# Performance work log

Hardware: AMD Instinct MI355X
Metric: run time of the kernel (lower is better)

Reference implementation:

```python
import jax, jax.numpy as jnp
import numpy as np

LN_EPS = 1e-5  # torch.nn.LayerNorm default


def setup_inputs() -> dict:
    key = jax.random.key(0)
    k1, k2 = jax.random.split(key)
    N, D_IN, D_OUT, G = 4096, 512, 512, 32
    x = jax.random.normal(k1, (N, D_IN), dtype=jnp.float32)
    ln_w = jnp.ones((D_IN,), dtype=jnp.float32)
    ln_b = jnp.zeros((D_IN,), dtype=jnp.float32)
    scale = 1.0 / (np.sqrt(D_IN) * np.sqrt(G))
    fouriercoeffs = jax.random.normal(k2, (2, D_OUT, D_IN, G), dtype=jnp.float32) * scale
    bias = jnp.zeros((1, D_OUT), dtype=jnp.float32)
    return {"x": x, "ln_w": ln_w, "ln_b": ln_b, "fouriercoeffs": fouriercoeffs, "bias": bias}


def reference(x, ln_w, ln_b, fouriercoeffs, bias):
    # LayerNorm over last dim
    mu = jnp.mean(x, axis=-1, keepdims=True)
    var = jnp.mean((x - mu) ** 2, axis=-1, keepdims=True)
    xn = (x - mu) * jax.lax.rsqrt(var + LN_EPS) * ln_w + ln_b
    G = fouriercoeffs.shape[-1]
    k = jnp.arange(1, G + 1, dtype=xn.dtype)           # [G]
    arg = xn[:, :, None] * k                            # [N, D_in, G]
    c = jnp.cos(arg)
    s = jnp.sin(arg)
    # contraction over (inputdim, gridsize) -> GEMM-shaped einsum
    y = jnp.einsum('big,oig->bo', c, fouriercoeffs[0])
    y = y + jnp.einsum('big,oig->bo', s, fouriercoeffs[1])
    y = y + bias
    return y
```

## Files before the change

kernel.cpp:

```cpp
#include <hip/hip_runtime.h>
#include <hip/hip_bf16.h>


#define N_ROWS 4096
#define D_IN   512
#define D_OUT  512
#define KT     16384
#define BM 128
#define BN 128
#define SPLITK 4

typedef short short8 __attribute__((ext_vector_type(8)));
typedef float float4v __attribute__((ext_vector_type(4)));

__device__ inline unsigned int pack2bf(float a, float b) {
    __hip_bfloat162 h = __float22bfloat162_rn(make_float2(a, b));
    union { __hip_bfloat162 h; unsigned int u; } cv;
    cv.h = h;
    return cv.u;
}

__device__ inline unsigned short bf16_1(float a) {
    union { float f; unsigned int u; } cv;
    cv.f = a;
    unsigned int r = (cv.u + 0x7fff + ((cv.u >> 16) & 1)) >> 16;
    return (unsigned short)r;
}

__global__ __launch_bounds__(256) void ln_stats(const float* __restrict__ x,
        float2* __restrict__ mu_rs) {
    const int t = threadIdx.x;
    const int row = blockIdx.x * 4 + (t >> 6);
    const int lane = t & 63;
    const float4* xr = (const float4*)(x + (size_t)row * D_IN);
    float4 a = xr[lane];
    float4 c = xr[lane + 64];
    float s = a.x + a.y + a.z + a.w + c.x + c.y + c.z + c.w;
    float q = a.x * a.x + a.y * a.y + a.z * a.z + a.w * a.w
            + c.x * c.x + c.y * c.y + c.z * c.z + c.w * c.w;
    #pragma unroll
    for (int off = 32; off > 0; off >>= 1) {
        s += __shfl_down(s, off, 64);
        q += __shfl_down(q, off, 64);
    }
    if (lane == 0) {
        float mu = s * (1.f / D_IN);
        float var = q * (1.f / D_IN) - mu * mu;
        mu_rs[row] = make_float2(mu, rsqrtf(var + 1e-5f));
    }
}

__global__ __launch_bounds__(256) void feat_seed(const float* __restrict__ x,
        const float* __restrict__ w, const float* __restrict__ b,
        const float2* __restrict__ mu_rs, float2* __restrict__ csT) {
    __shared__ float2 tile[64][66];
    const int t = threadIdx.x;
    const int r0 = blockIdx.x * 64, i0 = blockIdx.y * 64;
    const int rr = t >> 6;
    const int cc = t & 63;
    const float wv = w[i0 + cc], bv = b[i0 + cc];
    #pragma unroll
    for (int p = 0; p < 16; ++p) {
        const int row = r0 + p * 4 + rr;
        float v = x[(size_t)row * D_IN + i0 + cc];
        float2 mr = mu_rs[row];
        float xn = (v - mr.x) * mr.y * wv + bv;
        float sn, cn;
        __sincosf(xn, &sn, &cn);
        tile[cc][p * 4 + rr] = make_float2(cn, sn);
    }
    __syncthreads();
    #pragma unroll
    for (int p = 0; p < 16; ++p) {
        const int dim = p * 4 + rr;
        csT[(size_t)(i0 + dim) * N_ROWS + r0 + cc] = tile[dim][cc];
    }
}

__global__ __launch_bounds__(256) void cvt_kernel(const float* __restrict__ fc,
        unsigned short* __restrict__ Wb) {
    size_t e = ((size_t)blockIdx.x * 256 + threadIdx.x) * 8;
    const float4* in = (const float4*)(fc + e);
    float4 a = in[0];
    float4 c = in[1];
    uint4 o;
    o.x = pack2bf(a.x, a.y);
    o.y = pack2bf(a.z, a.w);
    o.z = pack2bf(c.x, c.y);
    o.w = pack2bf(c.z, c.w);
    *(uint4*)(Wb + e) = o;
}

__device__ inline void stage_feats(unsigned short* Abuf, float2 cs, int ttype,
                                   int frow, int ihalf) {
    const float c1 = cs.x, s1 = cs.y;
    const float c2 = c1 + c1;
    float prev = ttype ? 0.f : 1.f;
    float cur  = ttype ? s1 : c1;
    const int rbase = frow * 64;
    const int sw = frow & 7;
    unsigned int us[4];
    #pragma unroll
    for (int d = 0; d < 16; ++d) {
        float f0 = cur;
        float f1 = __builtin_fmaf(c2, cur, -prev);
        float f2 = __builtin_fmaf(c2, f1, -cur);
        prev = f1;
        cur = f2;
        us[d & 3] = pack2bf(f0, f1);
        if ((d & 3) == 3) {
            const int kc = ihalf * 4 + (d >> 2);
            *(uint4*)&Abuf[rbase + ((kc ^ sw) << 3)] =
                make_uint4(us[0], us[1], us[2], us[3]);
        }
    }
}

__global__ __launch_bounds__(256, 2) void fkan_gemm(const float2* __restrict__ csT,
        const unsigned short* __restrict__ Wb, unsigned short* __restrict__ pb) {
    __shared__ unsigned short As[2][BM * 64];
    __shared__ unsigned short Bs[2][BN * 64];
    const int t = threadIdx.x;
    const int row0 = blockIdx.x * BM;
    const int col0 = blockIdx.y * BN;
    const int kz = blockIdx.z;
    const int k0 = kz * 4096;
    const int i0 = kz * 128;
    const int frow = t & 127;
    const int ihalf = t >> 7;
    const int l = t & 63, wv = t >> 6;
    const int wm = (wv & 1) * 64, wn = (wv >> 1) * 64;
    const int lm = l & 15, lq = l >> 4;
    const int c8 = l & 7, s8 = l >> 3;
    const unsigned short* Bg0 = Wb + (size_t)(col0 + wv * 32 + c8) * KT + k0 + s8 * 8;
    const int swA = lm & 7;
    const int bBase = ((wn >> 3) + (lm >> 3)) * 512 + lq * 64 + (lm & 7) * 8;

    const float2* csBase = csT + (size_t)(i0 + ihalf) * N_ROWS + row0 + frow;

    float4v acc[4][4];
    #pragma unroll
    for (int i = 0; i < 4; ++i)
        #pragma unroll
        for (int j = 0; j < 4; ++j)
            acc[i][j] = (float4v){0.f, 0.f, 0.f, 0.f};

    #pragma unroll
    for (int j = 0; j < 4; ++j) {
        const unsigned short* gsrc = Bg0 + (size_t)(j * 8) * KT;
        unsigned short* ldst = &Bs[0][(wv * 4 + j) * 512];
        __builtin_amdgcn_global_load_lds(
            (const __attribute__((address_space(1))) unsigned int*)gsrc,
            (__attribute__((address_space(3))) unsigned int*)ldst, 16, 0, 0);
    }
    float2 cs = csBase[0];
    stage_feats(As[0], cs, 0, frow, ihalf);
    cs = csBase[2 * N_ROWS];
    __syncthreads();

    for (int iter = 0; iter < 128; ++iter) {
        const int p = iter & 1;
        if (iter < 127) {
            const int in = iter + 1;
            const int tt = in >> 6, ii = in & 63;
            const unsigned short* gb = Bg0 + (size_t)tt * D_OUT * KT + ii * 64;
            #pragma unroll
            for (int j = 0; j < 4; ++j) {
                const unsigned short* gsrc = gb + (size_t)(j * 8) * KT;
                unsigned short* ldst = &Bs[p ^ 1][(wv * 4 + j) * 512];
                __builtin_amdgcn_global_load_lds(
                    (const __attribute__((address_space(1))) unsigned int*)gsrc,
                    (__attribute__((address_space(3))) unsigned int*)ldst, 16, 0, 0);
            }
            stage_feats(As[p ^ 1], cs, tt, frow, ihalf);
        }
        if (iter < 126)
            cs = csBase[(size_t)(((iter + 2) & 63) * 2) * N_ROWS];
        #pragma unroll
        for (int h = 0; h < 2; ++h) {
            short8 af[4], bf[4];
            #pragma unroll
            for (int tm = 0; tm < 4; ++tm)
                af[tm] = *(const short8*)
                    &As[p][(wm + tm * 16 + lm) * 64 + (((h * 4 + lq) ^ swA) << 3)];
            #pragma unroll
            for (int tn = 0; tn < 4; ++tn)
                bf[tn] = *(const short8*)&Bs[p][bBase + tn * 1024 + h * 256];
            #pragma unroll
            for (int tm = 0; tm < 4; ++tm)
                #pragma unroll
                for (int tn = 0; tn < 4; ++tn)
                    acc[tm][tn] = __builtin_amdgcn_mfma_f32_16x16x32_bf16(
                        af[tm], bf[tn], acc[tm][tn], 0, 0, 0);
        }
        __syncthreads();
    }
    unsigned short* pc = pb + (size_t)kz * N_ROWS * D_OUT;
    #pragma unroll
    for (int tm = 0; tm < 4; ++tm)
        #pragma unroll
        for (int tn = 0; tn < 4; ++tn)
            #pragma unroll
            for (int r = 0; r < 4; ++r) {
                const int row = row0 + wm + tm * 16 + lq * 4 + r;
                const int col = col0 + wn + tn * 16 + lm;
                pc[(size_t)row * D_OUT + col] = bf16_1(acc[tm][tn][r]);
            }
}

__global__ __launch_bounds__(256) void reduce_kernel(const unsigned short* __restrict__ pb,
        const float* __restrict__ bias, float* __restrict__ out) {
    const size_t e = ((size_t)blockIdx.x * 256 + threadIdx.x) * 4;
    const int col = (int)(e & (D_OUT - 1));
    float4 s = *(const float4*)(bias + col);
    #pragma unroll
    for (int c = 0; c < SPLITK; ++c) {
        ushort4 u = *(const ushort4*)(pb + (size_t)c * N_ROWS * D_OUT + e);
        union { unsigned int u; float f; } f0, f1, f2, f3;
        f0.u = (unsigned int)u.x << 16;
        f1.u = (unsigned int)u.y << 16;
        f2.u = (unsigned int)u.z << 16;
        f3.u = (unsigned int)u.w << 16;
        s.x += f0.f; s.y += f1.f; s.z += f2.f; s.w += f3.f;
    }
    *(float4*)(out + e) = s;
}

extern "C" void kernel_launch(void* const* d_in, const int* in_sizes, int n_in,
                              void* d_out, int out_size, void* d_ws, size_t ws_size,
                              hipStream_t stream) {
    const float* x    = (const float*)d_in[0];
    const float* ln_w = (const float*)d_in[1];
    const float* ln_b = (const float*)d_in[2];
    const float* fc   = (const float*)d_in[3];
    const float* bias = (const float*)d_in[4];
    float* out = (float*)d_out;

    float2* csT = (float2*)d_ws;
    float2* mu_rs = (float2*)((char*)d_ws + (16u << 20));
    unsigned short* Wb = (unsigned short*)((char*)d_ws + (17u << 20));
    unsigned short* pbp = (unsigned short*)((char*)d_ws + (51u << 20));

    ln_stats<<<N_ROWS / 4, 256, 0, stream>>>(x, mu_rs);
    feat_seed<<<dim3(N_ROWS / 64, D_IN / 64), 256, 0, stream>>>(x, ln_w, ln_b, mu_rs, csT);
    cvt_kernel<<<8192, 256, 0, stream>>>(fc, Wb);
    fkan_gemm<<<dim3(N_ROWS / BM, D_OUT / BN, SPLITK), 256, 0, stream>>>(csT, Wb, pbp);
    reduce_kernel<<<2048, 256, 0, stream>>>(pbp, bias, out);
}
```

Measured before the change: 312.1 us.

## Triple-buffer B tiles, single-buffer A with early fragment reads and setprio

Restructures the GEMM main loop so B tiles are prefetched two iterations ahead into a three-slot LDS ring, while A uses a single LDS buffer. A fragments are read into registers before the barrier so the next A tile can be staged in place, and explicit vmcnt/lgkmcnt waits replace __syncthreads. MFMA blocks run under raised wave priority. The feat_seed transpose tile padding and indexing are also changed. The aim is to hide global load latency and cut LDS use per block, at the cost of more register pressure from holding both h-halves of fragments and of hand-tuned wait counts that could be fragile.

```diff
diff --git a/kernel.cpp b/kernel.cpp
--- a/kernel.cpp
+++ b/kernel.cpp
@@ -53,7 +53,7 @@
 __global__ __launch_bounds__(256) void feat_seed(const float* __restrict__ x,
         const float* __restrict__ w, const float* __restrict__ b,
         const float2* __restrict__ mu_rs, float2* __restrict__ csT) {
-    __shared__ float2 tile[64][66];
+    __shared__ float2 tile[64][65];
     const int t = threadIdx.x;
     const int r0 = blockIdx.x * 64, i0 = blockIdx.y * 64;
     const int rr = t >> 6;
@@ -67,13 +67,13 @@
         float xn = (v - mr.x) * mr.y * wv + bv;
         float sn, cn;
         __sincosf(xn, &sn, &cn);
-        tile[cc][p * 4 + rr] = make_float2(cn, sn);
+        tile[p * 4 + rr][cc] = make_float2(cn, sn);
     }
     __syncthreads();
     #pragma unroll
     for (int p = 0; p < 16; ++p) {
         const int dim = p * 4 + rr;
-        csT[(size_t)(i0 + dim) * N_ROWS + r0 + cc] = tile[dim][cc];
+        csT[(size_t)(i0 + dim) * N_ROWS + r0 + cc] = tile[cc][dim];
     }
 }
 
@@ -116,10 +116,49 @@
     }
 }
 
+__device__ inline void gl_lds16(const unsigned short* gsrc, unsigned short* ldst) {
+    __builtin_amdgcn_global_load_lds(
+        (const __attribute__((address_space(1))) unsigned int*)gsrc,
+        (__attribute__((address_space(3))) unsigned int*)ldst, 16, 0, 0);
+}
+
+__device__ inline void read_af(const unsigned short* As, short8 (&af)[2][4],
+                               int wm, int lm, int lq, int swA) {
+    #pragma unroll
+    for (int h = 0; h < 2; ++h)
+        #pragma unroll
+        for (int tm = 0; tm < 4; ++tm)
+            af[h][tm] = *(const short8*)
+                &As[(wm + tm * 16 + lm) * 64 + (((h * 4 + lq) ^ swA) << 3)];
+}
+
+__device__ inline void read_bf(const unsigned short* Bp, short8 (&bf)[2][4],
+                               int bBase) {
+    #pragma unroll
+    for (int h = 0; h < 2; ++h)
+        #pragma unroll
+        for (int tn = 0; tn < 4; ++tn)
+            bf[h][tn] = *(const short8*)&Bp[bBase + tn * 1024 + h * 256];
+}
+
+__device__ inline void mfma_block(short8 (&af)[2][4], short8 (&bf)[2][4],
+                                  float4v (&acc)[4][4]) {
+    __builtin_amdgcn_s_setprio(1);
+    #pragma unroll
+    for (int h = 0; h < 2; ++h)
+        #pragma unroll
+        for (int tm = 0; tm < 4; ++tm)
+            #pragma unroll
+            for (int tn = 0; tn < 4; ++tn)
+                acc[tm][tn] = __builtin_amdgcn_mfma_f32_16x16x32_bf16(
+                    af[h][tm], bf[h][tn], acc[tm][tn], 0, 0, 0);
+    __builtin_amdgcn_s_setprio(0);
+}
+
 __global__ __launch_bounds__(256, 2) void fkan_gemm(const float2* __restrict__ csT,
         const unsigned short* __restrict__ Wb, unsigned short* __restrict__ pb) {
-    __shared__ unsigned short As[2][BM * 64];
-    __shared__ unsigned short Bs[2][BN * 64];
+    __shared__ unsigned short As[BM * 64];
+    __shared__ unsigned short Bs[3][BN * 64];
     const int t = threadIdx.x;
     const int row0 = blockIdx.x * BM;
     const int col0 = blockIdx.y * BN;
@@ -146,54 +185,65 @@
             acc[i][j] = (float4v){0.f, 0.f, 0.f, 0.f};
 
     #pragma unroll
-    for (int j = 0; j < 4; ++j) {
-        const unsigned short* gsrc = Bg0 + (size_t)(j * 8) * KT;
-        unsigned short* ldst = &Bs[0][(wv * 4 + j) * 512];
-        __builtin_amdgcn_global_load_lds(
-            (const __attribute__((address_space(1))) unsigned int*)gsrc,
-            (__attribute__((address_space(3))) unsigned int*)ldst, 16, 0, 0);
-    }
-    float2 cs = csBase[0];
-    stage_feats(As[0], cs, 0, frow, ihalf);
-    cs = csBase[2 * N_ROWS];
-    __syncthreads();
-
-    for (int iter = 0; iter < 128; ++iter) {
-        const int p = iter & 1;
-        if (iter < 127) {
-            const int in = iter + 1;
-            const int tt = in >> 6, ii = in & 63;
-            const unsigned short* gb = Bg0 + (size_t)tt * D_OUT * KT + ii * 64;
-            #pragma unroll
-            for (int j = 0; j < 4; ++j) {
-                const unsigned short* gsrc = gb + (size_t)(j * 8) * KT;
-                unsigned short* ldst = &Bs[p ^ 1][(wv * 4 + j) * 512];
-                __builtin_amdgcn_global_load_lds(
-                    (const __attribute__((address_space(1))) unsigned int*)gsrc,
-                    (__attribute__((address_space(3))) unsigned int*)ldst, 16, 0, 0);
+    for (int j = 0; j < 4; ++j)
+        gl_lds16(Bg0 + (size_t)(j * 8) * KT, &Bs[0][(wv * 4 + j) * 512]);
+    #pragma unroll
+    for (int j = 0; j < 4; ++j)
+        gl_lds16(Bg0 + 64 + (size_t)(j * 8) * KT, &Bs[1][(wv * 4 + j) * 512]);
+    {
+        float2 c0 = csBase[0];
+        float2 tmp = csBase[2 * N_ROWS];
+        stage_feats(As, c0, 0, frow, ihalf);
+        asm volatile("s_waitcnt vmcnt(4) lgkmcnt(0)" ::: "memory");
+        __builtin_amdgcn_s_barrier();
+        float2 csA = tmp;
+        int rd = 0, wr = 2;
+        for (int it = 0; it < 126; ++it) {
+            const unsigned short* Bp = &Bs[rd][0];
+            short8 af[2][4];
+            read_af(As, af, wm, lm, lq, swA);
+            {
+                const int in = it + 2;
+                const unsigned short* gb =
+                    Bg0 + (size_t)(in >> 6) * D_OUT * KT + (in & 63) * 64;
+                #pragma unroll
+                for (int j = 0; j < 4; ++j)
+                    gl_lds16(gb + (size_t)(j * 8) * KT, &Bs[wr][(wv * 4 + j) * 512]);
             }
-            stage_feats(As[p ^ 1], cs, tt, frow, ihalf);
-        }
-        if (iter < 126)
-            cs = csBase[(size_t)(((iter + 2) & 63) * 2) * N_ROWS];
-        #pragma unroll
-        for (int h = 0; h < 2; ++h) {
-            short8 af[4], bf[4];
-            #pragma unroll
-            for (int tm = 0; tm < 4; ++tm)
-                af[tm] = *(const short8*)
-                    &As[p][(wm + tm * 16 + lm) * 64 + (((h * 4 + lq) ^ swA) << 3)];
-            #pragma unroll
-            for (int tn = 0; tn < 4; ++tn)
-                bf[tn] = *(const short8*)&Bs[p][bBase + tn * 1024 + h * 256];
-            #pragma unroll
-            for (int tm = 0; tm < 4; ++tm)
-                #pragma unroll
-                for (int tn = 0; tn < 4; ++tn)
-                    acc[tm][tn] = __builtin_amdgcn_mfma_f32_16x16x32_bf16(
-                        af[tm], bf[tn], acc[tm][tn], 0, 0, 0);
-        }
-        __syncthreads();
+            asm volatile("s_waitcnt lgkmcnt(0)" ::: "memory");
+            __builtin_amdgcn_s_barrier();
+            float2 csN = csBase[(size_t)(((it + 2) & 63) * 2) * N_ROWS];
+            stage_feats(As, csA, (it + 1) >> 6, frow, ihalf);
+            csA = csN;
+            short8 bf[2][4];
+            read_bf(Bp, bf, bBase);
+            mfma_block(af, bf, acc);
+            asm volatile("s_waitcnt vmcnt(5) lgkmcnt(0)" ::: "memory");
+            __builtin_amdgcn_s_barrier();
+            rd = (rd == 2) ? 0 : rd + 1;
+            wr = (wr == 2) ? 0 : wr + 1;
+        }
+        {
+            const unsigned short* Bp = &Bs[0][0];
+            short8 af[2][4];
+            read_af(As, af, wm, lm, lq, swA);
+            asm volatile("s_waitcnt lgkmcnt(0)" ::: "memory");
+            __builtin_amdgcn_s_barrier();
+            stage_feats(As, csA, 1, frow, ihalf);
+            short8 bf[2][4];
+            read_bf(Bp, bf, bBase);
+            mfma_block(af, bf, acc);
+            asm volatile("s_waitcnt vmcnt(0) lgkmcnt(0)" ::: "memory");
+            __builtin_amdgcn_s_barrier();
+        }
+        {
+            const unsigned short* Bp = &Bs[1][0];
+            short8 af[2][4];
+            read_af(As, af, wm, lm, lq, swA);
+            short8 bf[2][4];
+            read_bf(Bp, bf, bBase);
+            mfma_block(af, bf, acc);
+        }
     }
     unsigned short* pc = pb + (size_t)kz * N_ROWS * D_OUT;
     #pragma unroll
```

Result: faster. 288.7 us (-7.5%).
